# Performance work log

Hardware: AMD Instinct MI355X
Metric: run time of the kernel (lower is better)

## Reference

```python
import jax, jax.numpy as jnp
import numpy as np

HIDDEN = 512
EXP = 2048  # hidden * expansion_factor(4)

def _glorot(key, shape):
    fan_in = shape[0]
    return jax.random.normal(key, shape, dtype=jnp.float32) / np.sqrt(fan_in)

def setup_inputs() -> dict:
    key = jax.random.key(0)
    ks = jax.random.split(key, 6)
    B, S = 4, 4096
    return {
        "x": jax.random.normal(ks[0], (B, S, HIDDEN), dtype=jnp.float32),
        "W_in1": _glorot(ks[1], (HIDDEN, EXP)),
        "b_in1": jnp.zeros((EXP,), jnp.float32),
        "W_in2": _glorot(ks[2], (HIDDEN, EXP)),
        "b_in2": jnp.zeros((EXP,), jnp.float32),
        "W_z": _glorot(ks[3], (EXP, EXP)),
        "b_z": jnp.zeros((EXP,), jnp.float32),
        "W_h": _glorot(ks[4], (EXP, EXP)),
        "b_h": jnp.zeros((EXP,), jnp.float32),
        "W_out": _glorot(ks[5], (EXP, HIDDEN)),
        "b_out": jnp.zeros((HIDDEN,), jnp.float32),
    }

def _min_gru(x_in, W_z, b_z, W_h, b_h):
    # minGRU: h_t = (1 - z_t) * h_{t-1} + z_t * h_tilde_t, h_0 = 0
    z = jax.nn.sigmoid(jnp.einsum("bse,ef->bsf", x_in, W_z) + b_z)
    h_tilde = jnp.einsum("bse,ef->bsf", x_in, W_h) + b_h
    a = 1.0 - z          # decay coeff
    b = z * h_tilde      # input term
    def combine(c1, c2):
        a1, b1 = c1
        a2, b2 = c2
        return (a1 * a2, b1 * a2 + b2)
    _, h = jax.lax.associative_scan(combine, (a, b), axis=1)
    return h

def reference(x, W_in1, b_in1, W_in2, b_in2, W_z, b_z, W_h, b_h, W_out, b_out):
    x_in = jax.nn.silu(jnp.einsum("bsd,de->bse", x, W_in1) + b_in1)
    x_skip = jax.nn.silu(jnp.einsum("bsd,de->bse", x, W_in2) + b_in2)
    h = _min_gru(x_in, W_z, b_z, W_h, b_h)
    return jnp.einsum("bse,ed->bsd", x_skip + h, W_out) + b_out
```

## Files before the change

### kernel.cpp

```cpp
#include <hip/hip_runtime.h>
#include <hip/hip_bf16.h>


typedef __bf16 bf16x8 __attribute__((ext_vector_type(8)));
typedef __bf16 bf16x4 __attribute__((ext_vector_type(4)));
typedef float  f32x4  __attribute__((ext_vector_type(4)));

#define DEVINL __device__ __forceinline__

DEVINL void async_ld16(const __bf16* g, __bf16* l) {
    __builtin_amdgcn_global_load_lds(
        (const __attribute__((address_space(1))) void*)g,
        (__attribute__((address_space(3))) void*)l, 16, 0, 0);
}

DEVINL float fsigmoid(float v) { return 1.0f / (1.0f + __expf(-v)); }

struct KLoopSM { __bf16 A[2][128 * 32]; __bf16 B[2][128 * 32]; };

template <int MODE>
__global__ __launch_bounds__(256)
void gemm_bt(const __bf16* __restrict__ A, const __bf16* __restrict__ Bt,
             const float* __restrict__ bias, const float* __restrict__ bias2,
             void* __restrict__ out, void* __restrict__ out2, int N, int K,
             int bps, int seg_stride, int row_off)
{
    __shared__ union SM {
        KLoopSM kl;
        __bf16 ct[64 * 136];
        float  ctf[32 * 132];
    } sm;
    const int tid = threadIdx.x;
    const int bx = blockIdx.x;
    const int seg = bx / bps;
    const int within = bx - seg * bps;
    const int gm0 = row_off + seg * seg_stride + within * 128;
    const int om0 = bx * 128;
    const int n0 = blockIdx.y * 128;

    const int c0 = tid, c1 = tid + 256;
    const int r0 = c0 >> 2, k0 = (c0 & 3) ^ ((c0 >> 3) & 3);
    const int r1 = c1 >> 2, k1 = (c1 & 3) ^ ((c1 >> 3) & 3);
    const __bf16* Ag0 = A  + (size_t)(gm0 + r0) * K + k0 * 8;
    const __bf16* Ag1 = A  + (size_t)(gm0 + r1) * K + k1 * 8;
    const __bf16* Bg0 = Bt + (size_t)(n0 + r0) * K + k0 * 8;
    const __bf16* Bg1 = Bt + (size_t)(n0 + r1) * K + k1 * 8;

    const int lane = tid & 63;
    const int wave = tid >> 6;
    const int wrow = (wave >> 1) * 64;
    const int wcol = (wave & 1) * 64;
    const int quad = lane >> 4;
    const int r = lane & 15;
    const int swz = (quad ^ ((r >> 1) & 3)) * 8;

    f32x4 acc[4][4] = {};

    const int T = K >> 5;
    async_ld16(Ag0, sm.kl.A[0] + c0 * 8);
    async_ld16(Ag1, sm.kl.A[0] + c1 * 8);
    async_ld16(Bg0, sm.kl.B[0] + c0 * 8);
    async_ld16(Bg1, sm.kl.B[0] + c1 * 8);

    for (int t = 0; t < T; ++t) {
        const int cur = t & 1;
        if (t + 1 < T) {
            const int kt = (t + 1) << 5;
            async_ld16(Ag0 + kt, sm.kl.A[cur ^ 1] + c0 * 8);
            async_ld16(Ag1 + kt, sm.kl.A[cur ^ 1] + c1 * 8);
            async_ld16(Bg0 + kt, sm.kl.B[cur ^ 1] + c0 * 8);
            async_ld16(Bg1 + kt, sm.kl.B[cur ^ 1] + c1 * 8);
            asm volatile("s_waitcnt vmcnt(4)\n\ts_barrier" ::: "memory");
        } else {
            asm volatile("s_waitcnt vmcnt(0)\n\ts_barrier" ::: "memory");
        }

        const __bf16* ap = sm.kl.A[cur] + (wrow + r) * 32 + swz;
        const __bf16* bp = sm.kl.B[cur] + (wcol + r) * 32 + swz;
        bf16x8 af[4], bf_[4];
#pragma unroll
        for (int i = 0; i < 4; ++i) af[i] = *(const bf16x8*)(ap + i * 512);
#pragma unroll
        for (int i = 0; i < 4; ++i) bf_[i] = *(const bf16x8*)(bp + i * 512);
#pragma unroll
        for (int i = 0; i < 4; ++i)
#pragma unroll
            for (int j = 0; j < 4; ++j)
                acc[i][j] = __builtin_amdgcn_mfma_f32_16x16x32_bf16(
                    af[i], bf_[j], acc[i][j], 0, 0, 0);

        asm volatile("s_waitcnt lgkmcnt(0)\n\ts_barrier" ::: "memory");
    }

    if (MODE == 3) {
        float bvj[4];
#pragma unroll
        for (int j = 0; j < 4; ++j)
            bvj[j] = bias[n0 + wcol + j * 16 + r];
#pragma unroll
        for (int p = 0; p < 4; ++p) {
#pragma unroll
            for (int j = 0; j < 4; ++j)
#pragma unroll
                for (int k = 0; k < 4; ++k)
                    sm.ctf[((wave >> 1) * 16 + quad * 4 + k) * 132 +
                           (wcol + j * 16 + r)] = acc[p][j][k] + bvj[j];
            __syncthreads();
#pragma unroll
            for (int q = 0; q < 4; ++q) {
                const int chunk = q * 256 + tid;
                const int trow = chunk >> 5;
                const int tc4 = (chunk & 31) * 4;
                const f32x4 vv = *(const f32x4*)(sm.ctf + trow * 132 + tc4);
                const int grow = om0 + (trow >> 4) * 64 + p * 16 + (trow & 15);
                *(f32x4*)((float*)out + (size_t)grow * N + n0 + tc4) = vv;
            }
            __syncthreads();
        }
    } else {
        const bool lo = n0 < 2048;
        __bf16* dst;
        int cb;
        size_t stride;
        if (MODE == 0) {
            dst = lo ? (__bf16*)out : (__bf16*)out2;
            cb = lo ? n0 : n0 - 2048;
            stride = 2048;
        } else {
            dst = (__bf16*)out;
            cb = n0;
            stride = (size_t)N;
        }
        float bvj[4];
#pragma unroll
        for (int j = 0; j < 4; ++j) {
            const int gc = n0 + wcol + j * 16 + r;
            bvj[j] = lo ? bias[gc] : bias2[gc - 2048];
        }
#pragma unroll
        for (int p = 0; p < 2; ++p) {
#pragma unroll
            for (int ii = 0; ii < 2; ++ii) {
                const int i = 2 * p + ii;
#pragma unroll
                for (int j = 0; j < 4; ++j)
#pragma unroll
                    for (int k = 0; k < 4; ++k) {
                        const float v = acc[i][j][k] + bvj[j];
                        const __bf16 o = (MODE == 0) ? (__bf16)(v * fsigmoid(v))
                                                     : (__bf16)v;
                        sm.ct[((wave >> 1) * 32 + ii * 16 + quad * 4 + k) * 136 +
                              (wcol + j * 16 + r)] = o;
                    }
            }
            __syncthreads();
#pragma unroll
            for (int q = 0; q < 4; ++q) {
                const int chunk = q * 256 + tid;
                const int trow = chunk >> 4;
                const int tc = (chunk & 15) * 8;
                const bf16x8 vv = *(const bf16x8*)(sm.ct + trow * 136 + tc);
                const int grow = om0 + (trow >> 5) * 64 + p * 32 + (trow & 31);
                *(bf16x8*)(dst + (size_t)grow * stride + cb + tc) = vv;
            }
            __syncthreads();
        }
    }
}

#define SSEG 32
#define SCOLS 32
__global__ __launch_bounds__(1024)
void scan_kernel(const __bf16* __restrict__ raw, __bf16* __restrict__ xskip,
                 float* __restrict__ carry, int CS, int S, int t0, int first)
{
    __shared__ float Als[SSEG][SCOLS];
    __shared__ float Bls[SSEG][SCOLS];
    const int lane = threadIdx.x & (SCOLS - 1);
    const int w = threadIdx.x >> 5;
    const int nb8 = gridDim.x >> 3;
    const int lin = (blockIdx.x & 7) * nb8 + (blockIdx.x >> 3);
    const int gpb = 2048 / SCOLS;
    const int batch = lin / gpb;
    const int col = (lin - batch * gpb) * SCOLS + lane;
    const int L = CS / SSEG;
    const int tbeg = w * L;

    const size_t rbase = ((size_t)batch * CS + tbeg) * 4096 + col;

    float av[32], bv[32];
    float A = 1.0f, Bv = 0.0f;
    {
        size_t idx = rbase;
#pragma unroll
        for (int t = 0; t < 32; ++t, idx += 4096) {
            const float z = fsigmoid((float)raw[idx]);
            const float b = z * (float)raw[idx + 2048];
            const float a = 1.0f - z;
            av[t] = a;
            bv[t] = b;
            Bv = a * Bv + b;
            A *= a;
        }
    }
    Als[w][lane] = A;
    Bls[w][lane] = Bv;
    __syncthreads();

    const int ch = batch * 2048 + col;
    float h = first ? 0.0f : carry[ch];
    for (int s = 0; s < w; ++s)
        h = Als[s][lane] * h + Bls[s][lane];
    if (w == SSEG - 1)
        carry[ch] = A * h + Bv;

    {
        size_t gidx = ((size_t)batch * S + t0 + tbeg) * 2048 + col;
#pragma unroll
        for (int t = 0; t < 32; ++t, gidx += 2048) {
            h = av[t] * h + bv[t];
            xskip[gidx] = (__bf16)((float)xskip[gidx] + h);
        }
    }
}

__global__ __launch_bounds__(256)
void conv_f32_bf16(const float* __restrict__ x, __bf16* __restrict__ y, int n4)
{
    const int i = blockIdx.x * 256 + threadIdx.x;
    if (i >= n4) return;
    const float4 v = ((const float4*)x)[i];
    bf16x4 o;
    o[0] = (__bf16)v.x; o[1] = (__bf16)v.y; o[2] = (__bf16)v.z; o[3] = (__bf16)v.w;
    ((bf16x4*)y)[i] = o;
}

__global__ __launch_bounds__(256)
void transpose_bf16(const float* __restrict__ W, __bf16* __restrict__ Wt, int K, int N)
{
    __shared__ float tile[32][33];
    const int tx = threadIdx.x & 31;
    const int ty = threadIdx.x >> 5;
    const int nb = blockIdx.x * 32;
    const int kb = blockIdx.y * 32;
#pragma unroll
    for (int i = 0; i < 32; i += 8)
        tile[ty + i][tx] = W[(size_t)(kb + ty + i) * N + nb + tx];
    __syncthreads();
#pragma unroll
    for (int i = 0; i < 32; i += 8)
        Wt[(size_t)(nb + ty + i) * K + kb + tx] = (__bf16)tile[tx][ty + i];
}

extern "C" void kernel_launch(void* const* d_in, const int* in_sizes, int n_in,
                              void* d_out, int out_size, void* d_ws, size_t ws_size,
                              hipStream_t stream)
{
    const float* x     = (const float*)d_in[0];
    const float* W_in1 = (const float*)d_in[1];
    const float* b_in1 = (const float*)d_in[2];
    const float* W_in2 = (const float*)d_in[3];
    const float* b_in2 = (const float*)d_in[4];
    const float* W_z   = (const float*)d_in[5];
    const float* b_z   = (const float*)d_in[6];
    const float* W_h   = (const float*)d_in[7];
    const float* b_h   = (const float*)d_in[8];
    const float* W_out = (const float*)d_in[9];
    const float* b_out = (const float*)d_in[10];

    const int B = 4, S = 4096, H = 512, E = 2048;
    const int M = B * S;
    const int CS = 1024;
    const int NC = S / CS;
    const int MC = B * CS;

    const size_t MiB = 1024 * 1024;
    const size_t NEEDED = 183 * MiB;
    if (ws_size < NEEDED) return;

    char* ws = (char*)d_ws;
    __bf16* xb    = (__bf16*)(ws + 0);
    __bf16* rawzh = (__bf16*)(ws + 0);
    float*  carry = (float*) (ws + 32 * MiB);
    __bf16* xin   = (__bf16*)(ws + 33 * MiB);
    __bf16* xskip = (__bf16*)(ws + 97 * MiB);
    __bf16* Wt12  = (__bf16*)(ws + 161 * MiB);
    __bf16* Wtzh  = (__bf16*)(ws + 165 * MiB);
    __bf16* Wto   = (__bf16*)(ws + 181 * MiB);

    conv_f32_bf16<<<(M * H / 4 + 255) / 256, 256, 0, stream>>>(x, xb, M * H / 4);
    transpose_bf16<<<dim3(E / 32, H / 32), 256, 0, stream>>>(W_in1, Wt12, H, E);
    transpose_bf16<<<dim3(E / 32, H / 32), 256, 0, stream>>>(W_in2, Wt12 + (size_t)E * H, H, E);
    transpose_bf16<<<dim3(E / 32, E / 32), 256, 0, stream>>>(W_z, Wtzh, E, E);
    transpose_bf16<<<dim3(E / 32, E / 32), 256, 0, stream>>>(W_h, Wtzh + (size_t)E * E, E, E);
    transpose_bf16<<<dim3(H / 32, E / 32), 256, 0, stream>>>(W_out, Wto, E, H);

    gemm_bt<0><<<dim3(M / 128, 2 * E / 128), 256, 0, stream>>>(
        xb, Wt12, b_in1, b_in2, xin, xskip, 2 * E, H, M / 128, 0, 0);

    for (int c = 0; c < NC; ++c) {
        const int row_off = c * CS;
        gemm_bt<4><<<dim3(MC / 128, 2 * E / 128), 256, 0, stream>>>(
            xin, Wtzh, b_z, b_h, rawzh, nullptr, 2 * E, E, CS / 128, S, row_off);
        scan_kernel<<<(B * E) / SCOLS, 1024, 0, stream>>>(
            rawzh, xskip, carry, CS, S, row_off, c == 0);
    }

    gemm_bt<3><<<dim3(M / 128, H / 128), 256, 0, stream>>>(
        xskip, Wto, b_out, nullptr, (float*)d_out, nullptr, H, E, M / 128, 0, 0);
}
```

Before: 662.6 us.

## Add 256x256-tile 512-thread GEMM with 4-stage async pipeline for input and gate GEMMs

```diff
diff --git a/kernel.cpp b/kernel.cpp
--- a/kernel.cpp
+++ b/kernel.cpp
@@ -15,6 +15,137 @@
 }
 
 DEVINL float fsigmoid(float v) { return 1.0f / (1.0f + __expf(-v)); }
+
+template <int MODE>
+__global__ __launch_bounds__(512, 2)
+void gemm3(const __bf16* __restrict__ A, const __bf16* __restrict__ Bt,
+           const float* __restrict__ bias, const float* __restrict__ bias2,
+           void* __restrict__ out, void* __restrict__ out2, int N, int K,
+           int bps, int seg_stride, int row_off)
+{
+    __shared__ union SM3 {
+        __bf16 kl[4][2][256 * 32];
+        __bf16 ct[64 * 264];
+    } sm;
+    const int tid = threadIdx.x;
+    const int bx = blockIdx.x;
+    const int seg = bx / bps;
+    const int within = bx - seg * bps;
+    const int gm0 = row_off + seg * seg_stride + within * 256;
+    const int om0 = bx * 256;
+    const int n0 = blockIdx.y * 256;
+
+    const int c0 = tid, c1 = tid + 512;
+    const int r0 = c0 >> 2, k0 = (c0 & 3) ^ ((c0 >> 3) & 3);
+    const int r1 = c1 >> 2, k1 = (c1 & 3) ^ ((c1 >> 3) & 3);
+    const __bf16* Ag0 = A  + (size_t)(gm0 + r0) * K + k0 * 8;
+    const __bf16* Ag1 = A  + (size_t)(gm0 + r1) * K + k1 * 8;
+    const __bf16* Bg0 = Bt + (size_t)(n0 + r0) * K + k0 * 8;
+    const __bf16* Bg1 = Bt + (size_t)(n0 + r1) * K + k1 * 8;
+
+    const int lane = tid & 63;
+    const int wave = tid >> 6;
+    const int wm = wave >> 2;
+    const int wn = wave & 3;
+    const int quad = lane >> 4;
+    const int r = lane & 15;
+    const int swz = (quad ^ ((r >> 1) & 3)) * 8;
+
+    f32x4 acc[8][4] = {};
+
+    const int T = K >> 5;
+
+    auto stage = [&](int t, int b) {
+        const int kt = t << 5;
+        async_ld16(Ag0 + kt, sm.kl[b][0] + c0 * 8);
+        async_ld16(Ag1 + kt, sm.kl[b][0] + c1 * 8);
+        async_ld16(Bg0 + kt, sm.kl[b][1] + c0 * 8);
+        async_ld16(Bg1 + kt, sm.kl[b][1] + c1 * 8);
+    };
+
+    stage(0, 0);
+    stage(1, 1);
+    stage(2, 2);
+
+    for (int t = 0; t < T; ++t) {
+        if (t + 2 < T) {
+            asm volatile("s_waitcnt vmcnt(8)\n\ts_barrier" ::: "memory");
+        } else if (t + 1 < T) {
+            asm volatile("s_waitcnt vmcnt(4)\n\ts_barrier" ::: "memory");
+        } else {
+            asm volatile("s_waitcnt vmcnt(0)\n\ts_barrier" ::: "memory");
+        }
+        if (t + 3 < T) stage(t + 3, (t + 3) & 3);
+
+        const __bf16* ap = sm.kl[t & 3][0] + (wm * 128 + r) * 32 + swz;
+        const __bf16* bp = sm.kl[t & 3][1] + (wn * 64 + r) * 32 + swz;
+        bf16x8 af[8], bf_[4];
+#pragma unroll
+        for (int m = 0; m < 8; ++m) af[m] = *(const bf16x8*)(ap + m * 512);
+#pragma unroll
+        for (int n = 0; n < 4; ++n) bf_[n] = *(const bf16x8*)(bp + n * 512);
+
+        __builtin_amdgcn_s_setprio(1);
+#pragma unroll
+        for (int m = 0; m < 8; ++m)
+#pragma unroll
+            for (int n = 0; n < 4; ++n)
+                acc[m][n] = __builtin_amdgcn_mfma_f32_16x16x32_bf16(
+                    af[m], bf_[n], acc[m][n], 0, 0, 0);
+        __builtin_amdgcn_s_setprio(0);
+    }
+
+    __syncthreads();
+
+    const bool lo = n0 < 2048;
+    __bf16* dst;
+    int cb;
+    size_t stride;
+    if (MODE == 0) {
+        dst = lo ? (__bf16*)out : (__bf16*)out2;
+        cb = lo ? n0 : n0 - 2048;
+        stride = 2048;
+    } else {
+        dst = (__bf16*)out;
+        cb = n0;
+        stride = (size_t)N;
+    }
+    float bvj[4];
+#pragma unroll
+    for (int nf = 0; nf < 4; ++nf) {
+        const int gc = n0 + wn * 64 + nf * 16 + r;
+        bvj[nf] = lo ? bias[gc] : bias2[gc - 2048];
+    }
+
+#pragma unroll
+    for (int p = 0; p < 4; ++p) {
+        if (wm == (p >> 1)) {
+            const int mb = (p & 1) * 4;
+#pragma unroll
+            for (int mm = 0; mm < 4; ++mm)
+#pragma unroll
+                for (int nf = 0; nf < 4; ++nf)
+#pragma unroll
+                    for (int k = 0; k < 4; ++k) {
+                        const float v = acc[mb + mm][nf][k] + bvj[nf];
+                        const __bf16 o = (MODE == 0) ? (__bf16)(v * fsigmoid(v))
+                                                     : (__bf16)v;
+                        sm.ct[(mm * 16 + quad * 4 + k) * 264 +
+                              (wn * 64 + nf * 16 + r)] = o;
+                    }
+        }
+        __syncthreads();
+#pragma unroll
+        for (int q = 0; q < 4; ++q) {
+            const int chunk = q * 512 + tid;
+            const int trow = chunk >> 5;
+            const int tc = (chunk & 31) * 8;
+            const bf16x8 vv = *(const bf16x8*)(sm.ct + trow * 264 + tc);
+            *(bf16x8*)(dst + (size_t)(om0 + p * 64 + trow) * stride + cb + tc) = vv;
+        }
+        __syncthreads();
+    }
+}
 
 struct KLoopSM { __bf16 A[2][128 * 32]; __bf16 B[2][128 * 32]; };
 
@@ -295,13 +426,13 @@
     transpose_bf16<<<dim3(E / 32, E / 32), 256, 0, stream>>>(W_h, Wtzh + (size_t)E * E, E, E);
     transpose_bf16<<<dim3(H / 32, E / 32), 256, 0, stream>>>(W_out, Wto, E, H);
 
-    gemm_bt<0><<<dim3(M / 128, 2 * E / 128), 256, 0, stream>>>(
-        xb, Wt12, b_in1, b_in2, xin, xskip, 2 * E, H, M / 128, 0, 0);
+    gemm3<0><<<dim3(M / 256, 2 * E / 256), 512, 0, stream>>>(
+        xb, Wt12, b_in1, b_in2, xin, xskip, 2 * E, H, M / 256, 0, 0);
 
     for (int c = 0; c < NC; ++c) {
         const int row_off = c * CS;
-        gemm_bt<4><<<dim3(MC / 128, 2 * E / 128), 256, 0, stream>>>(
-            xin, Wtzh, b_z, b_h, rawzh, nullptr, 2 * E, E, CS / 128, S, row_off);
+        gemm3<4><<<dim3(MC / 256, 2 * E / 256), 512, 0, stream>>>(
+            xin, Wtzh, b_z, b_h, rawzh, nullptr, 2 * E, E, CS / 256, S, row_off);
         scan_kernel<<<(B * E) / SCOLS, 1024, 0, stream>>>(
             rawzh, xskip, carry, CS, S, row_off, c == 0);
     }
```

Measured after the change: 607.2 us. 1.09x faster.
